# Performance work log

Measured on AMD Instinct MI355X. Metric: run time of the kernel, lower is better.

## Reference

```python
import jax, jax.numpy as jnp
import numpy as np

N_NODES = 50000
N_EDGES = 500000
D = 128
VOCAB = 10000
OUT = 64
LAYERS = 3
N_GRAPHS = 512


def setup_inputs() -> dict:
    key = jax.random.key(0)
    ks = jax.random.split(key, 10)
    nodes = jax.random.randint(ks[0], (N_NODES,), 0, VOCAB)
    edges = jax.random.randint(ks[1], (2, N_EDGES), 0, N_NODES)
    indices = jax.random.randint(ks[2], (N_NODES,), 0, N_GRAPHS)
    emb = jax.random.normal(ks[3], (VOCAB, D), dtype=jnp.float32) * 0.02
    W0 = jax.random.normal(ks[4], (LAYERS, D, D), dtype=jnp.float32) * (1.0 / np.sqrt(D))
    W1 = jax.random.normal(ks[5], (LAYERS, D, D), dtype=jnp.float32) * (1.0 / np.sqrt(D))
    W2 = jax.random.normal(ks[6], (LAYERS, D, D), dtype=jnp.float32) * (1.0 / np.sqrt(D))
    Wout = jax.random.normal(ks[7], (2 * D, OUT), dtype=jnp.float32) * (1.0 / np.sqrt(2 * D))
    bout = jnp.zeros((OUT,), dtype=jnp.float32)
    return {"nodes": nodes, "edges": edges, "indices": indices, "num_graphs": N_GRAPHS,
            "emb": emb, "W0": W0, "W1": W1, "W2": W2, "Wout": Wout, "bout": bout}


def reference(nodes, edges, indices, num_graphs, emb, W0, W1, W2, Wout, bout):
    n = nodes.shape[0]
    h = emb[nodes]  # [N, D]; Dropout(0.5) is identity in eval mode
    src, dst = edges[0], edges[1]
    seg = jnp.concatenate([dst, src])  # message destinations, [2E]
    deg = jax.ops.segment_sum(jnp.ones_like(seg, dtype=h.dtype), seg, num_segments=n)
    deg = jnp.maximum(deg, 1.0)[:, None]
    for l in range(W0.shape[0]):
        # per-edge linear on gathered endpoints (nn.Linear: x @ W.T)
        m = jnp.concatenate([h[src] @ W1[l].T, h[dst] @ W2[l].T], axis=0)  # [2E, D]
        msg = jax.ops.segment_sum(m, seg, num_segments=n) / deg  # scatter_mean
        h = jax.nn.relu(h @ W0[l].T + msg)
    # graph pooling: scatter_mean + scatter_max
    cnt = jax.ops.segment_sum(jnp.ones((n,), h.dtype), indices, num_segments=num_graphs)
    mean = jax.ops.segment_sum(h, indices, num_segments=num_graphs) / jnp.maximum(cnt, 1.0)[:, None]
    mx = jax.ops.segment_max(h, indices, num_segments=num_graphs)
    mx = jnp.where(jnp.isfinite(mx), mx, 0.0)  # empty segments -> 0 (torch_scatter default)
    v = jnp.concatenate([mean, mx], axis=1)  # [G, 2D]
    return v @ Wout + bout
```

## Files before the change

kernel.cpp:

```cpp
#include <hip/hip_runtime.h>
#include <hip/hip_bf16.h>

#define D 128
#define GRAPHS 512
#define OUTD 64

typedef _Float16 half4v __attribute__((ext_vector_type(4)));
typedef _Float16 half8v __attribute__((ext_vector_type(8)));
typedef float float4v __attribute__((ext_vector_type(4)));
typedef float float8v __attribute__((ext_vector_type(8)));
typedef unsigned short u16;

__global__ void hist_kernel(const int* __restrict__ edges, const int* __restrict__ indices,
                            int* cnt_in, int* cnt_out, int* gcnt,
                            u16* __restrict__ rank_in, u16* __restrict__ rank_out,
                            u16* __restrict__ grank, int E, int n) {
    int i = blockIdx.x * 256 + threadIdx.x;
    if (i < E) {
        int s = edges[i];
        int d = edges[E + i];
        rank_out[i] = (u16)atomicAdd(&cnt_out[s], 1);
        rank_in[i]  = (u16)atomicAdd(&cnt_in[d], 1);
    }
    if (i < n) grank[i] = (u16)atomicAdd(&gcnt[indices[i]], 1);
}

__global__ __launch_bounds__(256) void offsets_kernel(
    const int* __restrict__ c_in, int* __restrict__ o_in,
    const int* __restrict__ c_out, int* __restrict__ o_out,
    const int* __restrict__ c_g, int* __restrict__ o_g,
    int* totals, int n) {
    __shared__ int ws[8];
    int tid = threadIdx.x;
    int lane = tid & 63, wid = tid >> 6;
    int i = blockIdx.x * 256 + tid;

#define SCAN_ALLOC(cnt, off, total, len)                                   \
    do {                                                                   \
        int v_ = (i < (len)) ? (cnt)[i] : 0;                               \
        int orig_ = v_;                                                    \
        _Pragma("unroll") for (int d_ = 1; d_ < 64; d_ <<= 1) {            \
            int t_ = __shfl_up(v_, d_, 64);                                \
            if (lane >= d_) v_ += t_;                                      \
        }                                                                  \
        if (lane == 63) ws[wid] = v_;                                      \
        __syncthreads();                                                   \
        if (tid == 0) {                                                    \
            int s_ = 0;                                                    \
            for (int k_ = 0; k_ < 4; ++k_) { int t_ = ws[k_]; ws[k_] = s_; s_ += t_; } \
            ws[4] = atomicAdd((total), s_);                                \
        }                                                                  \
        __syncthreads();                                                   \
        if (i < (len)) (off)[i] = ws[4] + ws[wid] + v_ - orig_;            \
        __syncthreads();                                                   \
    } while (0)

    SCAN_ALLOC(c_in, o_in, &totals[0], n);
    SCAN_ALLOC(c_out, o_out, &totals[1], n);
    if (blockIdx.x < (GRAPHS + 255) / 256) SCAN_ALLOC(c_g, o_g, &totals[2], GRAPHS);
#undef SCAN_ALLOC
}

__global__ void mega_kernel(const int* __restrict__ nodes, const float* __restrict__ emb,
                            _Float16* __restrict__ h,
                            const int* __restrict__ edges, const int* __restrict__ indices,
                            const int* __restrict__ off_in, const int* __restrict__ off_out,
                            const int* __restrict__ goff,
                            const u16* __restrict__ rank_in, const u16* __restrict__ rank_out,
                            const u16* __restrict__ grank,
                            u16* __restrict__ csr_in, u16* __restrict__ csr_out,
                            u16* __restrict__ glist,
                            const float* __restrict__ W0, const float* __restrict__ W1,
                            const float* __restrict__ W2, _Float16* __restrict__ Wpk,
                            int E, int n) {
    int i = blockIdx.x * 256 + threadIdx.x;
    if (i < n * 16) {
        int v = i >> 4, q = i & 15;
        const float4* e4 = (const float4*)emb + (size_t)nodes[v] * 32 + q * 2;
        float4 f0 = e4[0];
        float4 f1 = e4[1];
        half8v o = {(_Float16)f0.x, (_Float16)f0.y, (_Float16)f0.z, (_Float16)f0.w,
                    (_Float16)f1.x, (_Float16)f1.y, (_Float16)f1.z, (_Float16)f1.w};
        ((half8v*)h)[i] = o;
    }
    if (i < E) {
        int s = edges[i];
        int d = edges[E + i];
        csr_in[off_in[d] + rank_in[i]]   = (u16)s;
        csr_out[off_out[s] + rank_out[i]] = (u16)d;
    }
    if (i < n)
        glist[goff[indices[i]] + grank[i]] = (u16)i;
    if (i < 36864) {
        int j4 = (i & 1) * 4;
        int t = i >> 1;
        int lane = t & 63; t >>= 6;
        int nf = t & 7;   t >>= 3;
        int ks = t & 3;   t >>= 2;
        int src = t % 3;
        int l = t / 3;
        const float* W = (src == 0 ? W0 : (src == 1 ? W1 : W2)) + l * D * D;
        int col = nf * 16 + (lane & 15);
        int k = ks * 32 + (lane >> 4) * 8 + j4;
        float4 f = *(const float4*)&W[col * D + k];
        half4v o = {(_Float16)f.x, (_Float16)f.y, (_Float16)f.z, (_Float16)f.w};
        _Float16* dst = Wpk + ((size_t)(((l * 3 + src) * 4 + ks) * 8 + nf) * 64 + lane) * 8 + j4;
        *(half4v*)dst = o;
    }
}

__global__ __launch_bounds__(256) void aggregate_kernel(
    const _Float16* __restrict__ h,
    const u16* __restrict__ csr_in, const int* __restrict__ off_in, const int* __restrict__ cnt_in,
    const u16* __restrict__ csr_out, const int* __restrict__ off_out, const int* __restrict__ cnt_out,
    _Float16* __restrict__ agg1, _Float16* __restrict__ agg2, int n) {
    int grp = threadIdx.x >> 4;
    int lane = threadIdx.x & 15;
    int v = blockIdx.x * 16 + grp;
    if (v >= n) return;
    int s1 = off_in[v], c1 = cnt_in[v];
    int s2 = off_out[v], c2 = cnt_out[v];
    float invd = 1.0f / fmaxf((float)(c1 + c2), 1.0f);
    const half8v* h8 = (const half8v*)h;

    float8v a1 = {0.f, 0.f, 0.f, 0.f, 0.f, 0.f, 0.f, 0.f};
    int i = 0;
    for (; i + 4 <= c1; i += 4) {
        int u0 = csr_in[s1 + i], u1 = csr_in[s1 + i + 1];
        int u2 = csr_in[s1 + i + 2], u3 = csr_in[s1 + i + 3];
        half8v p0 = h8[u0 * 16 + lane];
        half8v p1 = h8[u1 * 16 + lane];
        half8v p2 = h8[u2 * 16 + lane];
        half8v p3 = h8[u3 * 16 + lane];
        a1 += (__builtin_convertvector(p0, float8v) + __builtin_convertvector(p1, float8v)) +
              (__builtin_convertvector(p2, float8v) + __builtin_convertvector(p3, float8v));
    }
    for (; i < c1; ++i)
        a1 += __builtin_convertvector(h8[csr_in[s1 + i] * 16 + lane], float8v);

    float8v a2 = {0.f, 0.f, 0.f, 0.f, 0.f, 0.f, 0.f, 0.f};
    i = 0;
    for (; i + 4 <= c2; i += 4) {
        int u0 = csr_out[s2 + i], u1 = csr_out[s2 + i + 1];
        int u2 = csr_out[s2 + i + 2], u3 = csr_out[s2 + i + 3];
        half8v p0 = h8[u0 * 16 + lane];
        half8v p1 = h8[u1 * 16 + lane];
        half8v p2 = h8[u2 * 16 + lane];
        half8v p3 = h8[u3 * 16 + lane];
        a2 += (__builtin_convertvector(p0, float8v) + __builtin_convertvector(p1, float8v)) +
              (__builtin_convertvector(p2, float8v) + __builtin_convertvector(p3, float8v));
    }
    for (; i < c2; ++i)
        a2 += __builtin_convertvector(h8[csr_out[s2 + i] * 16 + lane], float8v);

    a1 *= invd;
    a2 *= invd;
    ((half8v*)agg1)[v * 16 + lane] = __builtin_convertvector(a1, half8v);
    ((half8v*)agg2)[v * 16 + lane] = __builtin_convertvector(a2, half8v);
}

__global__ __launch_bounds__(128) void transform_mfma(
    const _Float16* __restrict__ Xh, const _Float16* __restrict__ A1,
    const _Float16* __restrict__ A2, const _Float16* __restrict__ Wl,
    _Float16* __restrict__ Hout, int n) {
    __shared__ _Float16 Hs[64][136];
    int tid = threadIdx.x;
    int w = tid >> 6, lane = tid & 63;
    int rbase = blockIdx.x * 64 + w * 32;
    int m0 = lane & 15;
    int kg = lane >> 4;
    int r0 = min(rbase + m0, n - 1);
    int r1 = min(rbase + 16 + m0, n - 1);

    const _Float16* srcs[3] = {Xh, A1, A2};

    float4v acc[2][8];
#pragma unroll
    for (int mf = 0; mf < 2; ++mf)
#pragma unroll
        for (int nf = 0; nf < 8; ++nf) acc[mf][nf] = (float4v){0.f, 0.f, 0.f, 0.f};

#define LOAD_STEP(stp, A0v, A1v, Bv)                                              \
    do {                                                                          \
        const int src_ = (stp) >> 2, ks_ = (stp) & 3;                             \
        const _Float16* X_ = srcs[src_];                                          \
        A0v = *(const half8v*)(X_ + (size_t)r0 * D + ks_ * 32 + kg * 8);          \
        A1v = *(const half8v*)(X_ + (size_t)r1 * D + ks_ * 32 + kg * 8);          \
        const _Float16* wp_ = Wl + (size_t)((src_ * 4 + ks_) * 8) * 512 + lane * 8; \
        _Pragma("unroll") for (int nf_ = 0; nf_ < 8; ++nf_)                       \
            Bv[nf_] = *(const half8v*)(wp_ + nf_ * 512);                          \
    } while (0)

    half8v a0c, a1c, bc[8], a0n, a1n, bn[8];
    LOAD_STEP(0, a0c, a1c, bc);
#pragma unroll
    for (int step = 0; step < 12; ++step) {
        if (step < 11) LOAD_STEP(step + 1, a0n, a1n, bn);
#pragma unroll
        for (int nf = 0; nf < 8; ++nf) {
            acc[0][nf] = __builtin_amdgcn_mfma_f32_16x16x32_f16(a0c, bc[nf], acc[0][nf], 0, 0, 0);
            acc[1][nf] = __builtin_amdgcn_mfma_f32_16x16x32_f16(a1c, bc[nf], acc[1][nf], 0, 0, 0);
        }
        a0c = a0n; a1c = a1n;
#pragma unroll
        for (int nf = 0; nf < 8; ++nf) bc[nf] = bn[nf];
    }
#undef LOAD_STEP

#pragma unroll
    for (int mf = 0; mf < 2; ++mf)
#pragma unroll
        for (int nf = 0; nf < 8; ++nf)
#pragma unroll
            for (int r = 0; r < 4; ++r) {
                int row = w * 32 + mf * 16 + kg * 4 + r;
                int col = nf * 16 + m0;
                Hs[row][col] = (_Float16)fmaxf(acc[mf][nf][r], 0.0f);
            }
    __syncthreads();
#pragma unroll
    for (int it = 0; it < 8; ++it) {
        int id = tid + it * 128;
        int row = id >> 4, c8 = id & 15;
        int grow = blockIdx.x * 64 + row;
        if (grow < n)
            *(half8v*)(Hout + (size_t)grow * D + c8 * 8) = *(const half8v*)&Hs[row][c8 * 8];
    }
}

__global__ __launch_bounds__(128) void pool_head_kernel(
    const _Float16* __restrict__ h, const u16* __restrict__ glist,
    const int* __restrict__ goff, const int* __restrict__ gcnt,
    const float* __restrict__ Wout, const float* __restrict__ bout,
    float* __restrict__ out) {
    __shared__ float feat[2 * D];
    int g = blockIdx.x;
    int t = threadIdx.x;
    int s = goff[g], c = gcnt[g];
    float sum = 0.0f, mx = 0.0f;
    int i = 0;
    for (; i + 4 <= c; i += 4) {
        int v0 = glist[s + i], v1 = glist[s + i + 1];
        int v2 = glist[s + i + 2], v3 = glist[s + i + 3];
        float a = (float)h[(size_t)v0 * D + t];
        float b = (float)h[(size_t)v1 * D + t];
        float cc = (float)h[(size_t)v2 * D + t];
        float d = (float)h[(size_t)v3 * D + t];
        sum += (a + b) + (cc + d);
        mx = fmaxf(mx, fmaxf(fmaxf(a, b), fmaxf(cc, d)));
    }
    for (; i < c; ++i) {
        float a = (float)h[(size_t)glist[s + i] * D + t];
        sum += a;
        mx = fmaxf(mx, a);
    }
    feat[t] = sum / fmaxf((float)c, 1.0f);
    feat[D + t] = mx;
    __syncthreads();
    if (t < OUTD) {
        float acc = bout[t];
#pragma unroll 8
        for (int k = 0; k < 2 * D; ++k)
            acc = fmaf(feat[k], Wout[k * OUTD + t], acc);
        out[g * OUTD + t] = acc;
    }
}

extern "C" void kernel_launch(void* const* d_in, const int* in_sizes, int n_in,
                              void* d_out, int out_size, void* d_ws, size_t ws_size,
                              hipStream_t stream) {
    const int* nodes   = (const int*)d_in[0];
    const int* edges   = (const int*)d_in[1];
    const int* indices = (const int*)d_in[2];
    const float* emb  = (const float*)d_in[4];
    const float* W0   = (const float*)d_in[5];
    const float* W1   = (const float*)d_in[6];
    const float* W2   = (const float*)d_in[7];
    const float* Wout = (const float*)d_in[8];
    const float* bout = (const float*)d_in[9];
    float* out = (float*)d_out;

    const int n = in_sizes[0];
    const int E = in_sizes[1] / 2;

    char* ws = (char*)d_ws;
    size_t off = 0;
    auto alloc = [&](size_t bytes) -> char* {
        char* p = ws + off;
        off = (off + bytes + 255) & ~(size_t)255;
        return p;
    };
    int* cnt_in  = (int*)alloc(n * sizeof(int));
    int* cnt_out = (int*)alloc(n * sizeof(int));
    int* gcnt    = (int*)alloc(GRAPHS * sizeof(int));
    int* totals  = (int*)alloc(3 * sizeof(int));
    size_t zbytes = off;
    int* off_in  = (int*)alloc(n * sizeof(int));
    int* off_out = (int*)alloc(n * sizeof(int));
    int* goff    = (int*)alloc(GRAPHS * sizeof(int));
    u16* rank_in  = (u16*)alloc(E * sizeof(u16));
    u16* rank_out = (u16*)alloc(E * sizeof(u16));
    u16* grank    = (u16*)alloc(n * sizeof(u16));
    u16* glist   = (u16*)alloc(n * sizeof(u16));
    u16* csr_in  = (u16*)alloc(E * sizeof(u16));
    u16* csr_out = (u16*)alloc(E * sizeof(u16));
    _Float16* Wpk = (_Float16*)alloc(3 * 3 * 4 * 8 * 64 * 8 * sizeof(_Float16));
    _Float16* B0 = (_Float16*)alloc((size_t)n * D * sizeof(_Float16));
    _Float16* B1 = (_Float16*)alloc((size_t)n * D * sizeof(_Float16));
    _Float16* B2 = (_Float16*)alloc((size_t)n * D * sizeof(_Float16));
    (void)ws_size;

    hipMemsetAsync(d_ws, 0, zbytes, stream);

    int eblocks = (E + 255) / 256;
    hist_kernel<<<eblocks, 256, 0, stream>>>(edges, indices, cnt_in, cnt_out, gcnt,
                                             rank_in, rank_out, grank, E, n);
    int oblocks = (n + 255) / 256;
    offsets_kernel<<<oblocks, 256, 0, stream>>>(cnt_in, off_in, cnt_out, off_out,
                                                gcnt, goff, totals, n);
    int pblocks = (n * 16 + 255) / 256;
    mega_kernel<<<pblocks, 256, 0, stream>>>(nodes, emb, B0, edges, indices,
                                             off_in, off_out, goff,
                                             rank_in, rank_out, grank,
                                             csr_in, csr_out, glist, W0, W1, W2, Wpk, E, n);

    int ablocks = (n + 15) / 16;
    int tblocks = (n + 63) / 64;
    for (int l = 0; l < 3; ++l) {
        aggregate_kernel<<<ablocks, 256, 0, stream>>>(B0, csr_in, off_in, cnt_in,
                                                      csr_out, off_out, cnt_out, B1, B2, n);
        transform_mfma<<<tblocks, 128, 0, stream>>>(B0, B1, B2,
                                                    Wpk + (size_t)l * 3 * 4 * 8 * 512,
                                                    B0, n);
    }

    pool_head_kernel<<<GRAPHS, 128, 0, stream>>>(B0, glist, goff, gcnt, Wout, bout, out);
}
```

Before: 327.4 us.

## Privatize CSR histogram counters into 8 copies and fold hist into prep kernel

```diff
diff --git a/kernel.cpp b/kernel.cpp
--- a/kernel.cpp
+++ b/kernel.cpp
@@ -4,6 +4,7 @@
 #define D 128
 #define GRAPHS 512
 #define OUTD 64
+#define NC 8
 
 typedef _Float16 half4v __attribute__((ext_vector_type(4)));
 typedef _Float16 half8v __attribute__((ext_vector_type(8)));
@@ -12,68 +13,23 @@
 typedef unsigned short u16;
 
 __global__ void hist_kernel(const int* __restrict__ edges, const int* __restrict__ indices,
-                            int* cnt_in, int* cnt_out, int* gcnt,
+                            int* cnt_in8, int* cnt_out8, int* gcnt8,
                             u16* __restrict__ rank_in, u16* __restrict__ rank_out,
-                            u16* __restrict__ grank, int E, int n) {
-    int i = blockIdx.x * 256 + threadIdx.x;
-    if (i < E) {
-        int s = edges[i];
-        int d = edges[E + i];
-        rank_out[i] = (u16)atomicAdd(&cnt_out[s], 1);
-        rank_in[i]  = (u16)atomicAdd(&cnt_in[d], 1);
-    }
-    if (i < n) grank[i] = (u16)atomicAdd(&gcnt[indices[i]], 1);
-}
-
-__global__ __launch_bounds__(256) void offsets_kernel(
-    const int* __restrict__ c_in, int* __restrict__ o_in,
-    const int* __restrict__ c_out, int* __restrict__ o_out,
-    const int* __restrict__ c_g, int* __restrict__ o_g,
-    int* totals, int n) {
-    __shared__ int ws[8];
-    int tid = threadIdx.x;
-    int lane = tid & 63, wid = tid >> 6;
-    int i = blockIdx.x * 256 + tid;
-
-#define SCAN_ALLOC(cnt, off, total, len)                                   \
-    do {                                                                   \
-        int v_ = (i < (len)) ? (cnt)[i] : 0;                               \
-        int orig_ = v_;                                                    \
-        _Pragma("unroll") for (int d_ = 1; d_ < 64; d_ <<= 1) {            \
-            int t_ = __shfl_up(v_, d_, 64);                                \
-            if (lane >= d_) v_ += t_;                                      \
-        }                                                                  \
-        if (lane == 63) ws[wid] = v_;                                      \
-        __syncthreads();                                                   \
-        if (tid == 0) {                                                    \
-            int s_ = 0;                                                    \
-            for (int k_ = 0; k_ < 4; ++k_) { int t_ = ws[k_]; ws[k_] = s_; s_ += t_; } \
-            ws[4] = atomicAdd((total), s_);                                \
-        }                                                                  \
-        __syncthreads();                                                   \
-        if (i < (len)) (off)[i] = ws[4] + ws[wid] + v_ - orig_;            \
-        __syncthreads();                                                   \
-    } while (0)
-
-    SCAN_ALLOC(c_in, o_in, &totals[0], n);
-    SCAN_ALLOC(c_out, o_out, &totals[1], n);
-    if (blockIdx.x < (GRAPHS + 255) / 256) SCAN_ALLOC(c_g, o_g, &totals[2], GRAPHS);
-#undef SCAN_ALLOC
-}
-
-__global__ void mega_kernel(const int* __restrict__ nodes, const float* __restrict__ emb,
+                            u16* __restrict__ grank,
+                            const int* __restrict__ nodes, const float* __restrict__ emb,
                             _Float16* __restrict__ h,
-                            const int* __restrict__ edges, const int* __restrict__ indices,
-                            const int* __restrict__ off_in, const int* __restrict__ off_out,
-                            const int* __restrict__ goff,
-                            const u16* __restrict__ rank_in, const u16* __restrict__ rank_out,
-                            const u16* __restrict__ grank,
-                            u16* __restrict__ csr_in, u16* __restrict__ csr_out,
-                            u16* __restrict__ glist,
                             const float* __restrict__ W0, const float* __restrict__ W1,
                             const float* __restrict__ W2, _Float16* __restrict__ Wpk,
                             int E, int n) {
     int i = blockIdx.x * 256 + threadIdx.x;
+    int c = (i >> 8) & (NC - 1);
+    if (i < E) {
+        int s = edges[i];
+        int d = edges[E + i];
+        rank_out[i] = (u16)atomicAdd(&cnt_out8[c * n + s], 1);
+        rank_in[i]  = (u16)atomicAdd(&cnt_in8[c * n + d], 1);
+    }
+    if (i < n) grank[i] = (u16)atomicAdd(&gcnt8[c * GRAPHS + indices[i]], 1);
     if (i < n * 16) {
         int v = i >> 4, q = i & 15;
         const float4* e4 = (const float4*)emb + (size_t)nodes[v] * 32 + q * 2;
@@ -83,14 +39,6 @@
                     (_Float16)f1.x, (_Float16)f1.y, (_Float16)f1.z, (_Float16)f1.w};
         ((half8v*)h)[i] = o;
     }
-    if (i < E) {
-        int s = edges[i];
-        int d = edges[E + i];
-        csr_in[off_in[d] + rank_in[i]]   = (u16)s;
-        csr_out[off_out[s] + rank_out[i]] = (u16)d;
-    }
-    if (i < n)
-        glist[goff[indices[i]] + grank[i]] = (u16)i;
     if (i < 36864) {
         int j4 = (i & 1) * 4;
         int t = i >> 1;
@@ -107,6 +55,75 @@
         _Float16* dst = Wpk + ((size_t)(((l * 3 + src) * 4 + ks) * 8 + nf) * 64 + lane) * 8 + j4;
         *(half4v*)dst = o;
     }
+}
+
+__global__ __launch_bounds__(256) void offsets_kernel(
+    const int* __restrict__ cnt_in8, int* __restrict__ o8_in, int* __restrict__ off_in,
+    int* __restrict__ tot_in,
+    const int* __restrict__ cnt_out8, int* __restrict__ o8_out, int* __restrict__ off_out,
+    int* __restrict__ tot_out,
+    const int* __restrict__ gcnt8, int* __restrict__ o8_g, int* __restrict__ goff,
+    int* __restrict__ gtot,
+    int* totals, int n) {
+    __shared__ int ws[8];
+    int tid = threadIdx.x;
+    int lane = tid & 63, wid = tid >> 6;
+    int i = blockIdx.x * 256 + tid;
+
+#define SCAN8(cnt8, o8, off, tot_arr, total, len)                          \
+    do {                                                                   \
+        int c8_[NC]; int tot_ = 0;                                         \
+        if (i < (len)) {                                                   \
+            _Pragma("unroll") for (int k_ = 0; k_ < NC; ++k_) {            \
+                c8_[k_] = (cnt8)[k_ * (len) + i]; tot_ += c8_[k_];         \
+            }                                                              \
+        }                                                                  \
+        int v_ = tot_;                                                     \
+        _Pragma("unroll") for (int d_ = 1; d_ < 64; d_ <<= 1) {            \
+            int t_ = __shfl_up(v_, d_, 64);                                \
+            if (lane >= d_) v_ += t_;                                      \
+        }                                                                  \
+        if (lane == 63) ws[wid] = v_;                                      \
+        __syncthreads();                                                   \
+        if (tid == 0) {                                                    \
+            int s_ = 0;                                                    \
+            for (int k_ = 0; k_ < 4; ++k_) { int t_ = ws[k_]; ws[k_] = s_; s_ += t_; } \
+            ws[4] = atomicAdd((total), s_);                                \
+        }                                                                  \
+        __syncthreads();                                                   \
+        if (i < (len)) {                                                   \
+            int run_ = ws[4] + ws[wid] + v_ - tot_;                        \
+            (off)[i] = run_; (tot_arr)[i] = tot_;                          \
+            _Pragma("unroll") for (int k_ = 0; k_ < NC; ++k_) {            \
+                (o8)[k_ * (len) + i] = run_; run_ += c8_[k_];              \
+            }                                                              \
+        }                                                                  \
+        __syncthreads();                                                   \
+    } while (0)
+
+    SCAN8(cnt_in8, o8_in, off_in, tot_in, &totals[0], n);
+    SCAN8(cnt_out8, o8_out, off_out, tot_out, &totals[1], n);
+    if (blockIdx.x < 2) SCAN8(gcnt8, o8_g, goff, gtot, &totals[2], GRAPHS);
+#undef SCAN8
+}
+
+__global__ void fill_kernel(const int* __restrict__ edges, const int* __restrict__ indices,
+                            const int* __restrict__ o8_in, const int* __restrict__ o8_out,
+                            const int* __restrict__ o8_g,
+                            const u16* __restrict__ rank_in, const u16* __restrict__ rank_out,
+                            const u16* __restrict__ grank,
+                            u16* __restrict__ csr_in, u16* __restrict__ csr_out,
+                            u16* __restrict__ glist, int E, int n) {
+    int i = blockIdx.x * 256 + threadIdx.x;
+    int c = (i >> 8) & (NC - 1);
+    if (i < E) {
+        int s = edges[i];
+        int d = edges[E + i];
+        csr_in[o8_in[c * n + d] + rank_in[i]]   = (u16)s;
+        csr_out[o8_out[c * n + s] + rank_out[i]] = (u16)d;
+    }
+    if (i < n)
+        glist[o8_g[c * GRAPHS + indices[i]] + grank[i]] = (u16)i;
 }
 
 __global__ __launch_bounds__(256) void aggregate_kernel(
@@ -290,14 +307,20 @@
         off = (off + bytes + 255) & ~(size_t)255;
         return p;
     };
-    int* cnt_in  = (int*)alloc(n * sizeof(int));
-    int* cnt_out = (int*)alloc(n * sizeof(int));
-    int* gcnt    = (int*)alloc(GRAPHS * sizeof(int));
-    int* totals  = (int*)alloc(3 * sizeof(int));
+    int* cnt_in8  = (int*)alloc((size_t)NC * n * sizeof(int));
+    int* cnt_out8 = (int*)alloc((size_t)NC * n * sizeof(int));
+    int* gcnt8    = (int*)alloc(NC * GRAPHS * sizeof(int));
+    int* totals   = (int*)alloc(3 * sizeof(int));
     size_t zbytes = off;
+    int* o8_in   = (int*)alloc((size_t)NC * n * sizeof(int));
+    int* o8_out  = (int*)alloc((size_t)NC * n * sizeof(int));
+    int* o8_g    = (int*)alloc(NC * GRAPHS * sizeof(int));
     int* off_in  = (int*)alloc(n * sizeof(int));
     int* off_out = (int*)alloc(n * sizeof(int));
+    int* tot_in  = (int*)alloc(n * sizeof(int));
+    int* tot_out = (int*)alloc(n * sizeof(int));
     int* goff    = (int*)alloc(GRAPHS * sizeof(int));
+    int* gtot    = (int*)alloc(GRAPHS * sizeof(int));
     u16* rank_in  = (u16*)alloc(E * sizeof(u16));
     u16* rank_out = (u16*)alloc(E * sizeof(u16));
     u16* grank    = (u16*)alloc(n * sizeof(u16));
@@ -312,27 +335,28 @@
 
     hipMemsetAsync(d_ws, 0, zbytes, stream);
 
+    int hblocks = (n * 16 + 255) / 256;
+    hist_kernel<<<hblocks, 256, 0, stream>>>(edges, indices, cnt_in8, cnt_out8, gcnt8,
+                                             rank_in, rank_out, grank,
+                                             nodes, emb, B0, W0, W1, W2, Wpk, E, n);
+    int oblocks = (n + 255) / 256;
+    offsets_kernel<<<oblocks, 256, 0, stream>>>(cnt_in8, o8_in, off_in, tot_in,
+                                                cnt_out8, o8_out, off_out, tot_out,
+                                                gcnt8, o8_g, goff, gtot, totals, n);
     int eblocks = (E + 255) / 256;
-    hist_kernel<<<eblocks, 256, 0, stream>>>(edges, indices, cnt_in, cnt_out, gcnt,
-                                             rank_in, rank_out, grank, E, n);
-    int oblocks = (n + 255) / 256;
-    offsets_kernel<<<oblocks, 256, 0, stream>>>(cnt_in, off_in, cnt_out, off_out,
-                                                gcnt, goff, totals, n);
-    int pblocks = (n * 16 + 255) / 256;
-    mega_kernel<<<pblocks, 256, 0, stream>>>(nodes, emb, B0, edges, indices,
-                                             off_in, off_out, goff,
+    fill_kernel<<<eblocks, 256, 0, stream>>>(edges, indices, o8_in, o8_out, o8_g,
                                              rank_in, rank_out, grank,
-                                             csr_in, csr_out, glist, W0, W1, W2, Wpk, E, n);
+                                             csr_in, csr_out, glist, E, n);
 
     int ablocks = (n + 15) / 16;
     int tblocks = (n + 63) / 64;
     for (int l = 0; l < 3; ++l) {
-        aggregate_kernel<<<ablocks, 256, 0, stream>>>(B0, csr_in, off_in, cnt_in,
-                                                      csr_out, off_out, cnt_out, B1, B2, n);
+        aggregate_kernel<<<ablocks, 256, 0, stream>>>(B0, csr_in, off_in, tot_in,
+                                                      csr_out, off_out, tot_out, B1, B2, n);
         transform_mfma<<<tblocks, 128, 0, stream>>>(B0, B1, B2,
                                                     Wpk + (size_t)l * 3 * 4 * 8 * 512,
                                                     B0, n);
     }
 
-    pool_head_kernel<<<GRAPHS, 128, 0, stream>>>(B0, glist, goff, gcnt, Wout, bout, out);
-}
+    pool_head_kernel<<<GRAPHS, 128, 0, stream>>>(B0, glist, goff, gtot, Wout, bout, out);
+}
```

Measured after the change: 316.1 us. -3.4%, faster.

## Build CSR via range-partitioned shared-memory histograms instead of global atomics

Applied to the files above, without the earlier changes.

```diff
diff --git a/kernel.cpp b/kernel.cpp
--- a/kernel.cpp
+++ b/kernel.cpp
@@ -4,6 +4,8 @@
 #define D 128
 #define GRAPHS 512
 #define OUTD 64
+#define NS 64
+#define LRANGE 800
 
 typedef _Float16 half4v __attribute__((ext_vector_type(4)));
 typedef _Float16 half8v __attribute__((ext_vector_type(8)));
@@ -11,18 +13,97 @@
 typedef float float8v __attribute__((ext_vector_type(8)));
 typedef unsigned short u16;
 
-__global__ void hist_kernel(const int* __restrict__ edges, const int* __restrict__ indices,
-                            int* cnt_in, int* cnt_out, int* gcnt,
-                            u16* __restrict__ rank_in, u16* __restrict__ rank_out,
-                            u16* __restrict__ grank, int E, int n) {
-    int i = blockIdx.x * 256 + threadIdx.x;
-    if (i < E) {
-        int s = edges[i];
-        int d = edges[E + i];
-        rank_out[i] = (u16)atomicAdd(&cnt_out[s], 1);
-        rank_in[i]  = (u16)atomicAdd(&cnt_in[d], 1);
-    }
-    if (i < n) grank[i] = (u16)atomicAdd(&gcnt[indices[i]], 1);
+__global__ __launch_bounds__(256) void prep_kernel(
+    const int* __restrict__ edges, const int* __restrict__ indices,
+    int* __restrict__ cnt_in, int* __restrict__ cnt_out, int* __restrict__ gcnt,
+    const int* __restrict__ nodes, const float* __restrict__ emb,
+    _Float16* __restrict__ h,
+    const float* __restrict__ W0, const float* __restrict__ W1,
+    const float* __restrict__ W2, _Float16* __restrict__ Wpk,
+    int E, int n) {
+    int tid = threadIdx.x;
+    if (blockIdx.x < NS) {
+        __shared__ int lcnt[LRANGE];
+        int b = blockIdx.x;
+        int range = (n + NS - 1) / NS;
+        int lo = b * range, hi = min(lo + range, n), len = hi - lo;
+        const int* srcp = edges;
+        const int* dstp = edges + E;
+        int E4 = E >> 2;
+
+#define HIT(k) { unsigned r_ = (unsigned)((k) - lo); if (r_ < (unsigned)len) atomicAdd(&lcnt[r_], 1); }
+        for (int j = tid; j < len; j += 256) lcnt[j] = 0;
+        __syncthreads();
+        {
+            const int4* p4 = (const int4*)dstp;
+            for (int it = tid; it < E4; it += 256) {
+                int4 v = p4[it];
+                HIT(v.x) HIT(v.y) HIT(v.z) HIT(v.w)
+            }
+            for (int e = E4 * 4 + tid; e < E; e += 256) HIT(dstp[e])
+        }
+        __syncthreads();
+        for (int j = tid; j < len; j += 256) cnt_in[lo + j] = lcnt[j];
+        __syncthreads();
+        for (int j = tid; j < len; j += 256) lcnt[j] = 0;
+        __syncthreads();
+        {
+            const int4* p4 = (const int4*)srcp;
+            for (int it = tid; it < E4; it += 256) {
+                int4 v = p4[it];
+                HIT(v.x) HIT(v.y) HIT(v.z) HIT(v.w)
+            }
+            for (int e = E4 * 4 + tid; e < E; e += 256) HIT(srcp[e])
+        }
+        __syncthreads();
+        for (int j = tid; j < len; j += 256) cnt_out[lo + j] = lcnt[j];
+        __syncthreads();
+#undef HIT
+        int grange = (GRAPHS + NS - 1) / NS;
+        int glo = b * grange, ghi = min(glo + grange, GRAPHS), glen = ghi - glo;
+        for (int j = tid; j < glen; j += 256) lcnt[j] = 0;
+        __syncthreads();
+#define GHIT(k) { unsigned r_ = (unsigned)((k) - glo); if (r_ < (unsigned)glen) atomicAdd(&lcnt[r_], 1); }
+        {
+            const int4* p4 = (const int4*)indices;
+            int n4 = n >> 2;
+            for (int it = tid; it < n4; it += 256) {
+                int4 v = p4[it];
+                GHIT(v.x) GHIT(v.y) GHIT(v.z) GHIT(v.w)
+            }
+            for (int e = n4 * 4 + tid; e < n; e += 256) GHIT(indices[e])
+        }
+        __syncthreads();
+        for (int j = tid; j < glen; j += 256) gcnt[glo + j] = lcnt[j];
+#undef GHIT
+        return;
+    }
+    int i = (blockIdx.x - NS) * 256 + tid;
+    if (i < n * 16) {
+        int v = i >> 4, q = i & 15;
+        const float4* e4 = (const float4*)emb + (size_t)nodes[v] * 32 + q * 2;
+        float4 f0 = e4[0];
+        float4 f1 = e4[1];
+        half8v o = {(_Float16)f0.x, (_Float16)f0.y, (_Float16)f0.z, (_Float16)f0.w,
+                    (_Float16)f1.x, (_Float16)f1.y, (_Float16)f1.z, (_Float16)f1.w};
+        ((half8v*)h)[i] = o;
+    }
+    if (i < 36864) {
+        int j4 = (i & 1) * 4;
+        int t = i >> 1;
+        int lane = t & 63; t >>= 6;
+        int nf = t & 7;   t >>= 3;
+        int ks = t & 3;   t >>= 2;
+        int src = t % 3;
+        int l = t / 3;
+        const float* W = (src == 0 ? W0 : (src == 1 ? W1 : W2)) + l * D * D;
+        int col = nf * 16 + (lane & 15);
+        int k = ks * 32 + (lane >> 4) * 8 + j4;
+        float4 f = *(const float4*)&W[col * D + k];
+        half4v o = {(_Float16)f.x, (_Float16)f.y, (_Float16)f.z, (_Float16)f.w};
+        _Float16* dst = Wpk + ((size_t)(((l * 3 + src) * 4 + ks) * 8 + nf) * 64 + lane) * 8 + j4;
+        *(half4v*)dst = o;
+    }
 }
 
 __global__ __launch_bounds__(256) void offsets_kernel(
@@ -61,52 +142,62 @@
 #undef SCAN_ALLOC
 }
 
-__global__ void mega_kernel(const int* __restrict__ nodes, const float* __restrict__ emb,
-                            _Float16* __restrict__ h,
-                            const int* __restrict__ edges, const int* __restrict__ indices,
-                            const int* __restrict__ off_in, const int* __restrict__ off_out,
-                            const int* __restrict__ goff,
-                            const u16* __restrict__ rank_in, const u16* __restrict__ rank_out,
-                            const u16* __restrict__ grank,
-                            u16* __restrict__ csr_in, u16* __restrict__ csr_out,
-                            u16* __restrict__ glist,
-                            const float* __restrict__ W0, const float* __restrict__ W1,
-                            const float* __restrict__ W2, _Float16* __restrict__ Wpk,
-                            int E, int n) {
-    int i = blockIdx.x * 256 + threadIdx.x;
-    if (i < n * 16) {
-        int v = i >> 4, q = i & 15;
-        const float4* e4 = (const float4*)emb + (size_t)nodes[v] * 32 + q * 2;
-        float4 f0 = e4[0];
-        float4 f1 = e4[1];
-        half8v o = {(_Float16)f0.x, (_Float16)f0.y, (_Float16)f0.z, (_Float16)f0.w,
-                    (_Float16)f1.x, (_Float16)f1.y, (_Float16)f1.z, (_Float16)f1.w};
-        ((half8v*)h)[i] = o;
-    }
-    if (i < E) {
-        int s = edges[i];
-        int d = edges[E + i];
-        csr_in[off_in[d] + rank_in[i]]   = (u16)s;
-        csr_out[off_out[s] + rank_out[i]] = (u16)d;
-    }
-    if (i < n)
-        glist[goff[indices[i]] + grank[i]] = (u16)i;
-    if (i < 36864) {
-        int j4 = (i & 1) * 4;
-        int t = i >> 1;
-        int lane = t & 63; t >>= 6;
-        int nf = t & 7;   t >>= 3;
-        int ks = t & 3;   t >>= 2;
-        int src = t % 3;
-        int l = t / 3;
-        const float* W = (src == 0 ? W0 : (src == 1 ? W1 : W2)) + l * D * D;
-        int col = nf * 16 + (lane & 15);
-        int k = ks * 32 + (lane >> 4) * 8 + j4;
-        float4 f = *(const float4*)&W[col * D + k];
-        half4v o = {(_Float16)f.x, (_Float16)f.y, (_Float16)f.z, (_Float16)f.w};
-        _Float16* dst = Wpk + ((size_t)(((l * 3 + src) * 4 + ks) * 8 + nf) * 64 + lane) * 8 + j4;
-        *(half4v*)dst = o;
-    }
+__global__ __launch_bounds__(256) void fill_kernel(
+    const int* __restrict__ edges, const int* __restrict__ indices,
+    const int* __restrict__ off_in, const int* __restrict__ off_out,
+    const int* __restrict__ goff,
+    u16* __restrict__ csr_in, u16* __restrict__ csr_out, u16* __restrict__ glist,
+    int E, int n) {
+    __shared__ int cin[LRANGE];
+    __shared__ int cout[LRANGE];
+    __shared__ int cg[16];
+    int tid = threadIdx.x;
+    int b = blockIdx.x;
+    int range = (n + NS - 1) / NS;
+    int lo = b * range, hi = min(lo + range, n), len = hi - lo;
+    int grange = (GRAPHS + NS - 1) / NS;
+    int glo = b * grange, ghi = min(glo + grange, GRAPHS), glen = ghi - glo;
+    for (int j = tid; j < len; j += 256) { cin[j] = off_in[lo + j]; cout[j] = off_out[lo + j]; }
+    for (int j = tid; j < glen; j += 256) cg[j] = goff[glo + j];
+    __syncthreads();
+
+    const int* srcp = edges;
+    const int* dstp = edges + E;
+    int E4 = E >> 2;
+#define FIN(k, idx) { unsigned r_ = (unsigned)((k) - lo); if (r_ < (unsigned)len) { \
+        int p_ = atomicAdd(&cin[r_], 1); csr_in[p_] = (u16)srcp[idx]; } }
+    {
+        const int4* p4 = (const int4*)dstp;
+        for (int it = tid; it < E4; it += 256) {
+            int4 v = p4[it]; int e = it * 4;
+            FIN(v.x, e) FIN(v.y, e + 1) FIN(v.z, e + 2) FIN(v.w, e + 3)
+        }
+        for (int e = E4 * 4 + tid; e < E; e += 256) FIN(dstp[e], e)
+    }
+#undef FIN
+#define FOUT(k, idx) { unsigned r_ = (unsigned)((k) - lo); if (r_ < (unsigned)len) { \
+        int p_ = atomicAdd(&cout[r_], 1); csr_out[p_] = (u16)dstp[idx]; } }
+    {
+        const int4* p4 = (const int4*)srcp;
+        for (int it = tid; it < E4; it += 256) {
+            int4 v = p4[it]; int e = it * 4;
+            FOUT(v.x, e) FOUT(v.y, e + 1) FOUT(v.z, e + 2) FOUT(v.w, e + 3)
+        }
+        for (int e = E4 * 4 + tid; e < E; e += 256) FOUT(srcp[e], e)
+    }
+#undef FOUT
+#define FG(g, vv) { unsigned r_ = (unsigned)((g) - glo); if (r_ < (unsigned)glen) { \
+        int p_ = atomicAdd(&cg[r_], 1); glist[p_] = (u16)(vv); } }
+    {
+        const int4* p4 = (const int4*)indices;
+        int n4 = n >> 2;
+        for (int it = tid; it < n4; it += 256) {
+            int4 v = p4[it]; int e = it * 4;
+            FG(v.x, e) FG(v.y, e + 1) FG(v.z, e + 2) FG(v.w, e + 3)
+        }
+        for (int e = n4 * 4 + tid; e < n; e += 256) FG(indices[e], e)
+    }
+#undef FG
 }
 
 __global__ __launch_bounds__(256) void aggregate_kernel(
@@ -290,17 +381,14 @@
         off = (off + bytes + 255) & ~(size_t)255;
         return p;
     };
+    int* totals = (int*)alloc(3 * sizeof(int));
+    size_t zbytes = off;
     int* cnt_in  = (int*)alloc(n * sizeof(int));
     int* cnt_out = (int*)alloc(n * sizeof(int));
     int* gcnt    = (int*)alloc(GRAPHS * sizeof(int));
-    int* totals  = (int*)alloc(3 * sizeof(int));
-    size_t zbytes = off;
     int* off_in  = (int*)alloc(n * sizeof(int));
     int* off_out = (int*)alloc(n * sizeof(int));
     int* goff    = (int*)alloc(GRAPHS * sizeof(int));
-    u16* rank_in  = (u16*)alloc(E * sizeof(u16));
-    u16* rank_out = (u16*)alloc(E * sizeof(u16));
-    u16* grank    = (u16*)alloc(n * sizeof(u16));
     u16* glist   = (u16*)alloc(n * sizeof(u16));
     u16* csr_in  = (u16*)alloc(E * sizeof(u16));
     u16* csr_out = (u16*)alloc(E * sizeof(u16));
@@ -312,17 +400,14 @@
 
     hipMemsetAsync(d_ws, 0, zbytes, stream);
 
-    int eblocks = (E + 255) / 256;
-    hist_kernel<<<eblocks, 256, 0, stream>>>(edges, indices, cnt_in, cnt_out, gcnt,
-                                             rank_in, rank_out, grank, E, n);
+    int pblocks = NS + (n * 16 + 255) / 256;
+    prep_kernel<<<pblocks, 256, 0, stream>>>(edges, indices, cnt_in, cnt_out, gcnt,
+                                             nodes, emb, B0, W0, W1, W2, Wpk, E, n);
     int oblocks = (n + 255) / 256;
     offsets_kernel<<<oblocks, 256, 0, stream>>>(cnt_in, off_in, cnt_out, off_out,
                                                 gcnt, goff, totals, n);
-    int pblocks = (n * 16 + 255) / 256;
-    mega_kernel<<<pblocks, 256, 0, stream>>>(nodes, emb, B0, edges, indices,
-                                             off_in, off_out, goff,
-                                             rank_in, rank_out, grank,
-                                             csr_in, csr_out, glist, W0, W1, W2, Wpk, E, n);
+    fill_kernel<<<NS, 256, 0, stream>>>(edges, indices, off_in, off_out, goff,
+                                        csr_in, csr_out, glist, E, n);
 
     int ablocks = (n + 15) / 16;
     int tblocks = (n + 63) / 64;
```

Measured after the change: 1.173 ms. 3.58x slower.
